# Optimization experiments

Hardware: AMD Instinct MI355X
Metric: run time of the kernel (lower is better)

Reference implementation:

```python
import jax, jax.numpy as jnp
import numpy as np

NUM_EMBED = 1024
EMBED_DIM = 256
COMMIT_COEF = 0.25


def setup_inputs() -> dict:
    key = jax.random.key(0)
    k1, k2 = jax.random.split(key)
    input = jax.random.normal(k1, (16, EMBED_DIM, 64, 64), dtype=jnp.float32)
    codebook = jax.random.normal(k2, (NUM_EMBED, EMBED_DIM), dtype=jnp.float32)
    last_used = jnp.zeros((NUM_EMBED,), dtype=jnp.int32)
    return {"input": input, "codebook": codebook, "last_used": last_used}


def reference(input, codebook, last_used):
    # (B, D, H, W) -> (B, H, W, D) -> (N, D)
    x = jnp.moveaxis(input, 1, -1)
    batch_shape = x.shape[:-1]
    flat = x.reshape(-1, x.shape[-1])  # (N, D)

    # Squared euclidean distances; argmin is identical to argmin of torch.cdist
    # (monotone sqrt), computed as a GEMM for efficiency.
    d2 = (
        jnp.sum(flat * flat, axis=-1, keepdims=True)
        - 2.0 * (flat @ codebook.T)
        + jnp.sum(codebook * codebook, axis=-1)
    )  # (N, K)
    idxes = jnp.argmin(d2, axis=-1).reshape(batch_shape)  # (B, H, W)

    embed = codebook[idxes]                 # (B, H, W, D) gather
    embed = jnp.moveaxis(embed, -1, 1)      # (B, D, H, W)

    # replace_unused bookkeeping (scatter). With last_used starting at zero,
    # last_used >= replace_after never triggers, so no codebook rewrite occurs.
    is_used = jnp.zeros((NUM_EMBED,), dtype=bool).at[idxes.ravel()].set(True)
    new_last_used = jnp.where(is_used, jnp.int32(0), last_used + jnp.int32(1))

    sg = jax.lax.stop_gradient
    codebook_loss = jnp.mean((sg(embed) - input) ** 2)
    commitment_loss = jnp.mean((embed - sg(input)) ** 2)
    vq_loss = codebook_loss + COMMIT_COEF * commitment_loss

    return idxes, embed, vq_loss, new_last_used
```

## Files before the change

kernel.cpp:

```cpp
#include <hip/hip_runtime.h>

#define NUM_EMBED 1024
#define EMBED_DIM 256
#define SPATIAL 4096
#define NROWS 65536
#define EMBED_ELEMS 16777216
#define HMARGIN 0.05f

typedef _Float16 half8 __attribute__((ext_vector_type(8)));
typedef float f32x4 __attribute__((ext_vector_type(4)));

__device__ __forceinline__ unsigned fkey(float f) {
  unsigned u = __float_as_uint(f);
  return (u & 0x80000000u) ? ~u : (u | 0x80000000u);
}

#define UPD(V1, V2, I1, S, I)                            \
  { float _s = (S);                                      \
    if (_s < (V1)) { (V2) = (V1); (V1) = _s; (I1) = (I); } \
    else if (_s < (V2)) { (V2) = _s; } }

#define MERGE(V1A, V2A, I1A, V1B, V2B, I1B)                       \
  { if ((V1B) < (V1A)) { (V2A) = fminf((V1A), (V2B)); (V1A) = (V1B); (I1A) = (I1B); } \
    else { (V2A) = fminf((V2A), (V1B)); } }

__global__ __launch_bounds__(256) void k_init(const float* __restrict__ cb,
                                              int* __restrict__ used,
                                              int* __restrict__ flagcount,
                                              float* __restrict__ cnorm,
                                              _Float16* __restrict__ cb16) {
  int bid = blockIdx.x, tid = threadIdx.x;
  if (bid == 0) {
    used[tid] = 0; used[tid + 256] = 0; used[tid + 512] = 0; used[tid + 768] = 0;
    if (tid == 0) *flagcount = 0;
  } else if (bid <= 64) {
    int c = (bid - 1) * 16 + (tid >> 4);
    int l = tid & 15;
    const float4* p = (const float4*)(cb + c * EMBED_DIM + l * 16);
    float s = 0.f;
#pragma unroll
    for (int j = 0; j < 4; ++j) {
      float4 v = p[j];
      s += v.x * v.x + v.y * v.y + v.z * v.z + v.w * v.w;
    }
#pragma unroll
    for (int off = 1; off < 16; off <<= 1) s += __shfl_xor(s, off, 16);
    if (l == 0) cnorm[c] = s;
  } else {
    int gid = (bid - 65) * 256 + tid;
    int ch = gid >> 9;
    int rem = gid & 511;
    int ks = rem >> 6;
    int lg = (rem >> 4) & 3;
    int ln = rem & 15;
    int S = (ch * 16 + ln) * 256 + ks * 32 + lg * 8;
    const float4* src = (const float4*)(cb + S);
    float4 a = src[0], b = src[1];
    half8 h;
    h[0] = (_Float16)a.x; h[1] = (_Float16)a.y; h[2] = (_Float16)a.z; h[3] = (_Float16)a.w;
    h[4] = (_Float16)b.x; h[5] = (_Float16)b.y; h[6] = (_Float16)b.z; h[7] = (_Float16)b.w;
    *(half8*)(cb16 + gid * 8) = h;
  }
}

__global__ __launch_bounds__(256, 2) void k_score(const float* __restrict__ in,
                                                  const _Float16* __restrict__ cb16,
                                                  const float* __restrict__ cnorm,
                                                  float* __restrict__ out_idx,
                                                  int* __restrict__ idxi,
                                                  int* __restrict__ flagged,
                                                  int* __restrict__ flagcount,
                                                  int* __restrict__ used,
                                                  double* __restrict__ partials) {
  __shared__ _Float16 As[4][4096];
  __shared__ float cn_lds[1024];
  int tid = threadIdx.x;
  int lane = tid & 63;
  int wave = tid >> 6;
  int ln = lane & 15;
  int lg = lane >> 4;
  int r0 = blockIdx.x << 6;
  const float* Ain = in + ((r0 >> 12) * (EMBED_DIM * SPATIAL)) + (r0 & 4095);

  {
    char* scratch = (char*)As[0];
    int row = tid & 63;
    int kq = tid >> 6;
    const float* p0 = Ain + row;
#pragma unroll
    for (int j = 0; j < 8; ++j) {
      int kc = kq * 8 + j;
      half8 hv;
#pragma unroll
      for (int q = 0; q < 8; ++q) hv[q] = (_Float16)p0[(kc * 8 + q) * SPATIAL];
      *(half8*)(scratch + kc * 1024 + row * 16) = hv;
    }
#pragma unroll
    for (int i = 0; i < 4; ++i) cn_lds[tid + 256 * i] = 0.5f * cnorm[tid + 256 * i];
  }
  __syncthreads();
  half8 xf[8][4];
  {
    const char* scratch = (const char*)As[0];
#pragma unroll
    for (int ks = 0; ks < 8; ++ks)
#pragma unroll
      for (int nf = 0; nf < 4; ++nf)
        xf[ks][nf] = *(const half8*)(scratch + (ks * 4 + lg) * 1024 + (nf * 16 + ln) * 16);
  }
  __syncthreads();

  char* buf = (char*)As[0] + wave * 8192;
  const _Float16* src0 = cb16 + wave * 65536 + lane * 8;

  half8 stg[8];
#pragma unroll
  for (int i = 0; i < 8; ++i) stg[i] = *(const half8*)(src0 + i * 512);
#pragma unroll
  for (int i = 0; i < 8; ++i) *(half8*)(buf + i * 1024 + lane * 16) = stg[i];

  float sv1[4] = {3e38f, 3e38f, 3e38f, 3e38f};
  float sv2[4] = {3e38f, 3e38f, 3e38f, 3e38f};
  int si1[4] = {0, 0, 0, 0};
  int afo = lg * 256 + ln * 16;

#pragma unroll 1
  for (int c = 0; c < 16; ++c) {
    if (c < 15) {
      const _Float16* ps = src0 + (c + 1) * 4096;
#pragma unroll
      for (int i = 0; i < 8; ++i) stg[i] = *(const half8*)(ps + i * 512);
    }
    f32x4 acc[4] = {};
    __builtin_amdgcn_s_setprio(1);
#pragma unroll
    for (int ks = 0; ks < 8; ++ks) {
      half8 af = *(const half8*)(buf + ks * 1024 + afo);
#pragma unroll
      for (int nf = 0; nf < 4; ++nf)
        acc[nf] = __builtin_amdgcn_mfma_f32_16x16x32_f16(af, xf[ks][nf], acc[nf], 0, 0, 0);
    }
    __builtin_amdgcn_s_setprio(0);
    int cb0 = wave * 256 + c * 16;
    float cna[4];
    *(float4*)cna = *(const float4*)(cn_lds + cb0 + lg * 4);
    int ib0 = cb0 + lg * 4;
#pragma unroll
    for (int nf = 0; nf < 4; ++nf) {
      float v1a = cna[0] - acc[nf][0], v2a = 3e38f;
      int i1a = ib0;
#pragma unroll
      for (int r = 1; r < 4; ++r) UPD(v1a, v2a, i1a, cna[r] - acc[nf][r], ib0 + r);
      MERGE(sv1[nf], sv2[nf], si1[nf], v1a, v2a, i1a);
    }
    if (c < 15) {
#pragma unroll
      for (int i = 0; i < 8; ++i) *(half8*)(buf + i * 1024 + lane * 16) = stg[i];
    }
  }

  float sx = 0.f;
  if (wave == 0) {
#pragma unroll
    for (int ks = 0; ks < 8; ++ks)
#pragma unroll
      for (int nf = 0; nf < 4; ++nf)
#pragma unroll
        for (int q = 0; q < 8; ++q) {
          float v = (float)xf[ks][nf][q];
          sx += v * v;
        }
#pragma unroll
    for (int off = 1; off < 64; off <<= 1) sx += __shfl_xor(sx, off, 64);
  }

#pragma unroll
  for (int nf = 0; nf < 4; ++nf) {
#pragma unroll
    for (int off = 16; off < 64; off <<= 1) {
      float ov1 = __shfl_xor(sv1[nf], off);
      float ov2 = __shfl_xor(sv2[nf], off);
      int oi = __shfl_xor(si1[nf], off);
      if (ov1 < sv1[nf]) { sv2[nf] = fminf(sv1[nf], ov2); sv1[nf] = ov1; si1[nf] = oi; }
      else { sv2[nf] = fminf(sv2[nf], ov1); }
    }
  }

  __syncthreads();
  float* mv1 = (float*)As[0];
  float* mv2 = mv1 + 256;
  int* mi1 = (int*)(mv2 + 256);
  if (lg == 0) {
#pragma unroll
    for (int nf = 0; nf < 4; ++nf) {
      int slot = wave * 64 + nf * 16 + ln;
      mv1[slot] = sv1[nf]; mv2[slot] = sv2[nf]; mi1[slot] = si1[nf];
    }
  }
  __syncthreads();
  if (tid < 64) {
    float v1 = mv1[tid], v2 = mv2[tid];
    int i1 = mi1[tid];
#pragma unroll
    for (int w = 1; w < 4; ++w)
      MERGE(v1, v2, i1, mv1[w * 64 + tid], mv2[w * 64 + tid], mi1[w * 64 + tid]);
    int grow = r0 + tid;
    out_idx[grow] = (float)i1;
    idxi[grow] = i1;
    if (v2 - v1 < HMARGIN) {
      int p = atomicAdd(flagcount, 1);
      flagged[p] = grow;
    } else {
      used[i1] = 1;
    }
    float hsum = v1;
#pragma unroll
    for (int off = 1; off < 64; off <<= 1) hsum += __shfl_xor(hsum, off, 64);
    if (tid == 0)
      partials[blockIdx.x] = (double)sx + 2.0 * (double)hsum;
  }
}

__global__ __launch_bounds__(256) void k_cleanup(const float* __restrict__ in,
                                                 const float* __restrict__ cb,
                                                 const float* __restrict__ cnorm,
                                                 const int* __restrict__ flagged,
                                                 const int* __restrict__ flagcount,
                                                 float* __restrict__ out_idx,
                                                 int* __restrict__ idxi,
                                                 int* __restrict__ used) {
  __shared__ float xs[256];
  __shared__ unsigned long long red[4];
  int tid = threadIdx.x;
  int lane = tid & 63;
  int wave = tid >> 6;
  int sub = lane & 15;
  int cg = lane >> 4;
  int nf = *flagcount;
  const float4* cb4 = (const float4*)cb;
  for (int fi = blockIdx.x; fi < nf; fi += 2048) {
    int row = flagged[fi];
    int b = row >> 12, s = row & 4095;
    xs[tid] = in[b * (EMBED_DIM * SPATIAL) + tid * SPATIAL + s];
    __syncthreads();
    const float4* xs4 = (const float4*)xs;
    float4 x0 = xs4[sub], x1 = xs4[16 + sub], x2 = xs4[32 + sub], x3 = xs4[48 + sub];
    unsigned long long best = ~0ull;
    int c0 = wave * 256 + cg;
#pragma unroll 4
    for (int g = 0; g < 64; ++g) {
      int c = c0 + g * 4;
      const float4* crow = cb4 + c * 64 + sub;
      float4 d0 = crow[0], d1 = crow[16], d2 = crow[32], d3 = crow[48];
      float p = d0.x * x0.x + d0.y * x0.y + d0.z * x0.z + d0.w * x0.w;
      p += d1.x * x1.x + d1.y * x1.y + d1.z * x1.z + d1.w * x1.w;
      p += d2.x * x2.x + d2.y * x2.y + d2.z * x2.z + d2.w * x2.w;
      p += d3.x * x3.x + d3.y * x3.y + d3.z * x3.z + d3.w * x3.w;
#pragma unroll
      for (int off = 1; off < 16; off <<= 1) p += __shfl_xor(p, off);
      if (sub == 0) {
        float sc = cnorm[c] - 2.0f * p;
        unsigned long long k = ((unsigned long long)fkey(sc) << 32) | (unsigned)c;
        best = k < best ? k : best;
      }
    }
    {
      unsigned long long o = __shfl_xor(best, 16); best = o < best ? o : best;
      o = __shfl_xor(best, 32); best = o < best ? o : best;
    }
    if (lane == 0) red[wave] = best;
    __syncthreads();
    if (tid == 0) {
      unsigned long long bb = red[0];
#pragma unroll
      for (int w = 1; w < 4; ++w) { unsigned long long o = red[w]; bb = o < bb ? o : bb; }
      int idx = (int)(bb & 0xffffffffull);
      out_idx[row] = (float)idx;
      idxi[row] = idx;
      used[idx] = 1;
    }
    __syncthreads();
  }
}

__global__ __launch_bounds__(256) void k_gather(const float* __restrict__ cb,
                                                const int* __restrict__ idxi,
                                                float* __restrict__ embed_out) {
  __shared__ float E[32][257];
  __shared__ int idx_l[32];
  int tid = threadIdx.x;
  int lane = tid & 63;
  int wave = tid >> 6;
  int r0 = blockIdx.x << 5;
  int b = r0 >> 12;
  int s0 = r0 & 4095;
  if (tid < 32) idx_l[tid] = idxi[r0 + tid];
  __syncthreads();
  const float4* cb4 = (const float4*)cb;
#pragma unroll
  for (int jj = 0; jj < 8; ++jj) {
    int j = wave * 8 + jj;
    float4 v = cb4[idx_l[j] * 64 + lane];
    E[j][lane * 4 + 0] = v.x;
    E[j][lane * 4 + 1] = v.y;
    E[j][lane * 4 + 2] = v.z;
    E[j][lane * 4 + 3] = v.w;
  }
  __syncthreads();
  int s = lane & 31;
  int dpar = lane >> 5;
  float* outp = embed_out + b * (EMBED_DIM * SPATIAL) + s0 + s;
#pragma unroll 8
  for (int i = 0; i < 32; ++i) {
    int d = wave * 64 + i * 2 + dpar;
    outp[d * SPATIAL] = E[s][d];
  }
}

__global__ __launch_bounds__(256) void k_tail(const double* __restrict__ partials,
                                              const int* __restrict__ used,
                                              const int* __restrict__ last_used,
                                              float* __restrict__ out_loss,
                                              float* __restrict__ out_lu) {
  int tid = threadIdx.x;
  double s = 0.0;
  for (int i = tid; i < 1024; i += 256) s += partials[i];
#pragma unroll
  for (int off = 1; off < 64; off <<= 1) s += __shfl_xor(s, off, 64);
  __shared__ double sd[4];
  if ((tid & 63) == 0) sd[tid >> 6] = s;
  __syncthreads();
  if (tid == 0) {
    double total = sd[0] + sd[1] + sd[2] + sd[3];
    out_loss[0] = (float)(1.25 * total / (double)EMBED_ELEMS);
  }
  for (int i = tid; i < NUM_EMBED; i += 256)
    out_lu[i] = used[i] ? 0.0f : (float)(last_used[i] + 1);
}

extern "C" void kernel_launch(void* const* d_in, const int* in_sizes, int n_in,
                              void* d_out, int out_size, void* d_ws, size_t ws_size,
                              hipStream_t stream) {
  const float* in = (const float*)d_in[0];
  const float* cb = (const float*)d_in[1];
  const int* last_used = (const int*)d_in[2];

  float* out = (float*)d_out;
  float* out_idx = out;
  float* embed_out = out + NROWS;
  float* out_loss = embed_out + EMBED_ELEMS;
  float* out_lu = out_loss + 1;

  _Float16* cb16 = (_Float16*)d_ws;
  double* partials = (double*)(cb16 + NUM_EMBED * EMBED_DIM);
  int* flagged = (int*)(partials + 4096);
  int* flagcount = flagged + NROWS;
  int* idxi = flagcount + 16;
  int* used = idxi + NROWS;
  float* cnorm = (float*)(used + NUM_EMBED);

  hipLaunchKernelGGL(k_init, dim3(193), dim3(256), 0, stream, cb, used, flagcount, cnorm, cb16);
  hipLaunchKernelGGL(k_score, dim3(1024), dim3(256), 0, stream, in, cb16, cnorm, out_idx,
                     idxi, flagged, flagcount, used, partials);
  hipLaunchKernelGGL(k_cleanup, dim3(2048), dim3(256), 0, stream, in, cb, cnorm, flagged,
                     flagcount, out_idx, idxi, used);
  hipLaunchKernelGGL(k_gather, dim3(2048), dim3(256), 0, stream, cb, idxi, embed_out);
  hipLaunchKernelGGL(k_tail, dim3(1), dim3(256), 0, stream, partials, used, last_used,
                     out_loss, out_lu);
}
```

Measured before the change: 125.5 us.

## Double-buffer codebook tiles in LDS with two-deep register prefetch

The per-wave LDS staging buffer for codebook chunks is doubled into two ping-pong buffers, and two sets of staging registers keep global loads two chunks ahead. The loop is unrolled by two so one buffer is written while the other feeds the MFMAs, with the aim of hiding global load latency and LDS write stalls behind compute. In exchange, LDS use doubles (64KB for As) and register pressure rises from the second staging array, which may reduce occupancy under launch_bounds(256,2).

```diff
diff --git a/kernel.cpp b/kernel.cpp
--- a/kernel.cpp
+++ b/kernel.cpp
@@ -72,7 +72,7 @@
                                                   int* __restrict__ flagcount,
                                                   int* __restrict__ used,
                                                   double* __restrict__ partials) {
-  __shared__ _Float16 As[4][4096];
+  __shared__ _Float16 As[8][4096];
   __shared__ float cn_lds[1024];
   int tid = threadIdx.x;
   int lane = tid & 63;
@@ -110,54 +110,72 @@
   }
   __syncthreads();
 
-  char* buf = (char*)As[0] + wave * 8192;
+  char* B0 = (char*)As[0] + wave * 16384;
+  char* B1 = B0 + 8192;
   const _Float16* src0 = cb16 + wave * 65536 + lane * 8;
-
-  half8 stg[8];
-#pragma unroll
-  for (int i = 0; i < 8; ++i) stg[i] = *(const half8*)(src0 + i * 512);
-#pragma unroll
-  for (int i = 0; i < 8; ++i) *(half8*)(buf + i * 1024 + lane * 16) = stg[i];
 
   float sv1[4] = {3e38f, 3e38f, 3e38f, 3e38f};
   float sv2[4] = {3e38f, 3e38f, 3e38f, 3e38f};
   int si1[4] = {0, 0, 0, 0};
   int afo = lg * 256 + ln * 16;
 
+  half8 sa[8], sb[8];
+#pragma unroll
+  for (int i = 0; i < 8; ++i) sa[i] = *(const half8*)(src0 + i * 512);
+#pragma unroll
+  for (int i = 0; i < 8; ++i) sb[i] = *(const half8*)(src0 + 4096 + i * 512);
+#pragma unroll
+  for (int i = 0; i < 8; ++i) *(half8*)(B0 + i * 1024 + lane * 16) = sa[i];
+#pragma unroll
+  for (int i = 0; i < 8; ++i) sa[i] = *(const half8*)(src0 + 2 * 4096 + i * 512);
+
+#define COMPUTE_FOLD(P, C)                                                          \
+  {                                                                                 \
+    f32x4 acc[4] = {};                                                              \
+    __builtin_amdgcn_s_setprio(1);                                                  \
+    _Pragma("unroll") for (int ks = 0; ks < 8; ++ks) {                              \
+      half8 af = *(const half8*)((P) + ks * 1024 + afo);                            \
+      _Pragma("unroll") for (int nf = 0; nf < 4; ++nf)                              \
+          acc[nf] = __builtin_amdgcn_mfma_f32_16x16x32_f16(af, xf[ks][nf], acc[nf], \
+                                                           0, 0, 0);                \
+    }                                                                               \
+    __builtin_amdgcn_s_setprio(0);                                                  \
+    int cb0 = wave * 256 + (C)*16;                                                  \
+    float cna[4];                                                                   \
+    *(float4*)cna = *(const float4*)(cn_lds + cb0 + lg * 4);                        \
+    int ib0 = cb0 + lg * 4;                                                         \
+    _Pragma("unroll") for (int nf = 0; nf < 4; ++nf) {                              \
+      float v1a = cna[0] - acc[nf][0], v2a = 3e38f;                                 \
+      int i1a = ib0;                                                                \
+      _Pragma("unroll") for (int r = 1; r < 4; ++r)                                 \
+          UPD(v1a, v2a, i1a, cna[r] - acc[nf][r], ib0 + r);                         \
+      MERGE(sv1[nf], sv2[nf], si1[nf], v1a, v2a, i1a);                              \
+    }                                                                               \
+  }
+
 #pragma unroll 1
-  for (int c = 0; c < 16; ++c) {
-    if (c < 15) {
-      const _Float16* ps = src0 + (c + 1) * 4096;
-#pragma unroll
-      for (int i = 0; i < 8; ++i) stg[i] = *(const half8*)(ps + i * 512);
-    }
-    f32x4 acc[4] = {};
-    __builtin_amdgcn_s_setprio(1);
-#pragma unroll
-    for (int ks = 0; ks < 8; ++ks) {
-      half8 af = *(const half8*)(buf + ks * 1024 + afo);
-#pragma unroll
-      for (int nf = 0; nf < 4; ++nf)
-        acc[nf] = __builtin_amdgcn_mfma_f32_16x16x32_f16(af, xf[ks][nf], acc[nf], 0, 0, 0);
-    }
-    __builtin_amdgcn_s_setprio(0);
-    int cb0 = wave * 256 + c * 16;
-    float cna[4];
-    *(float4*)cna = *(const float4*)(cn_lds + cb0 + lg * 4);
-    int ib0 = cb0 + lg * 4;
-#pragma unroll
-    for (int nf = 0; nf < 4; ++nf) {
-      float v1a = cna[0] - acc[nf][0], v2a = 3e38f;
-      int i1a = ib0;
-#pragma unroll
-      for (int r = 1; r < 4; ++r) UPD(v1a, v2a, i1a, cna[r] - acc[nf][r], ib0 + r);
-      MERGE(sv1[nf], sv2[nf], si1[nf], v1a, v2a, i1a);
-    }
-    if (c < 15) {
-#pragma unroll
-      for (int i = 0; i < 8; ++i) *(half8*)(buf + i * 1024 + lane * 16) = stg[i];
-    }
-  }
+  for (int j = 0; j < 8; ++j) {
+    int c0 = 2 * j;
+#pragma unroll
+    for (int i = 0; i < 8; ++i) *(half8*)(B1 + i * 1024 + lane * 16) = sb[i];
+    if (j < 7) {
+      const _Float16* ps = src0 + (2 * j + 3) * 4096;
+#pragma unroll
+      for (int i = 0; i < 8; ++i) sb[i] = *(const half8*)(ps + i * 512);
+    }
+    COMPUTE_FOLD(B0, c0);
+    if (j < 7) {
+#pragma unroll
+      for (int i = 0; i < 8; ++i) *(half8*)(B0 + i * 1024 + lane * 16) = sa[i];
+    }
+    if (j < 6) {
+      const _Float16* ps = src0 + (2 * j + 4) * 4096;
+#pragma unroll
+      for (int i = 0; i < 8; ++i) sa[i] = *(const half8*)(ps + i * 512);
+    }
+    COMPUTE_FOLD(B1, c0 + 1);
+  }
+#undef COMPUTE_FOLD
 
   float sx = 0.f;
   if (wave == 0) {
```

Measured after the change: 136.6 us. 8.9% more time.
